# Performance work log

Hardware: AMD Instinct MI355X
Metric: run time of the kernel (lower is better)

## Reference

```python
import jax, jax.numpy as jnp
import numpy as np


def _spline(t, x):
    """Natural cubic spline second derivatives. t: (T,), x: (T, N, D)."""
    T = t.shape[0]
    h = jnp.diff(t)  # (T-1,)
    main = jnp.concatenate([jnp.ones((1,), t.dtype), 2.0 * (h[:-1] + h[1:]), jnp.ones((1,), t.dtype)])
    lower = jnp.concatenate([h[:-1], jnp.zeros((1,), t.dtype)])
    upper = jnp.concatenate([jnp.zeros((1,), t.dtype), h[1:]])
    A = jnp.diag(main) + jnp.diag(lower, -1) + jnp.diag(upper, 1)  # (T, T) tridiagonal, natural BCs
    slopes = (x[1:] - x[:-1]) / h[:, None, None]
    rhs = jnp.concatenate([jnp.zeros_like(x[:1]), 6.0 * (slopes[1:] - slopes[:-1]), jnp.zeros_like(x[:1])], 0)
    M = jnp.linalg.solve(A, rhs.reshape(T, -1)).reshape(x.shape)  # (T, N, D)
    return h, M


def setup_inputs() -> dict:
    key = jax.random.key(0)
    ks = jax.random.split(key, 8)
    B, Amax, T, D, E, H = 32, 64, 16, 10, 128, 512
    t = jnp.arange(T, dtype=jnp.float32)
    x = jax.random.normal(ks[0], (B, Amax, T, D), jnp.float32)
    mask = jax.random.randint(ks[1], (B, Amax), 0, 2) > 0

    def lin(k, o, i):
        k1, k2 = jax.random.split(k)
        s = 1.0 / float(np.sqrt(i))  # torch nn.Linear default init
        return (jax.random.uniform(k1, (o, i), jnp.float32, -s, s),
                jax.random.uniform(k2, (o,), jnp.float32, -s, s))

    W_embed, b_embed = lin(ks[2], E, D)
    W0, b0 = lin(ks[3], H, E)
    W1, b1 = lin(ks[4], H, H)
    W2, b2 = lin(ks[5], H, H)
    W3, b3 = lin(ks[6], E * D, H)
    return dict(t=t, x=x, mask=mask, W_embed=W_embed, b_embed=b_embed,
                W0=W0, b0=b0, W1=W1, b1=b1, W2=W2, b2=b2, W3=W3, b3=b3)


def reference(t, x, mask, W_embed, b_embed, W0, b0, W1, b1, W2, b2, W3, b3):
    B, Amax, T, D = x.shape
    E = W_embed.shape[0]
    xs = x.reshape(B * Amax, T, D).transpose(1, 0, 2)  # (T, N, D)
    h, M = _spline(t, xs)

    def dX_dt(s):
        # derivative of the natural cubic spline at scalar time s -> (N, D)
        i = jnp.clip(jnp.searchsorted(t, s, side='right') - 1, 0, T - 2)
        u = s - t[i]
        hi = h[i]
        b = (xs[i + 1] - xs[i]) / hi - hi * (2.0 * M[i] + M[i + 1]) / 6.0
        return b + M[i] * u + (M[i + 1] - M[i]) * (u * u) / (2.0 * hi)

    def f(z):
        # CDEFunc: linear-relu x3, linear, tanh, view (N, E, D)
        y = jax.nn.relu(z @ W0.T + b0)
        y = jax.nn.relu(y @ W1.T + b1)
        y = jax.nn.relu(y @ W2.T + b2)
        y = jnp.tanh(y @ W3.T + b3)
        return y.reshape(z.shape[0], E, D)

    def vf(s, z):
        # VectorField: f(z) @ dX_dt(s)  -> (N, E)
        return jnp.einsum('ned,nd->ne', f(z), dX_dt(s))

    # spline evaluated at the first knot is just the first observation
    z0 = xs[0] @ W_embed.T + b_embed  # (N, E)

    def step(z, ts):
        # torchdiffeq 'rk4' fixed-step solver (3/8-rule, rk4_alt_step_func)
        t0, t1 = ts
        hs = t1 - t0
        k1 = vf(t0, z)
        k2 = vf(t0 + hs / 3.0, z + hs * k1 / 3.0)
        k3 = vf(t0 + 2.0 * hs / 3.0, z + hs * (k2 - k1 / 3.0))
        k4 = vf(t1, z + hs * (k1 - k2 + k3))
        return z + hs * (k1 + 3.0 * (k2 + k3) + k4) / 8.0, None

    zT, _ = jax.lax.scan(step, z0, (t[:-1], t[1:]))
    # masked-out agents get an all-zero embedding (as in the torch scatter)
    return zT.reshape(B, Amax, E) * mask[..., None].astype(zT.dtype)
```

## Files before the change

kernel.cpp:

```cpp
#include <hip/hip_runtime.h>
#include <hip/hip_bf16.h>


typedef __attribute__((ext_vector_type(4))) float f32x4;
typedef __attribute__((ext_vector_type(8))) short s16x8;

#define N_AG  2048
#define D_IN  10
#define NPTS  46
#define RROWS 8

#define OFF_W0P 0
#define OFF_W1P (128 * 512)
#define OFF_W2P (OFF_W1P + 512 * 512)
#define OFF_W3P (OFF_W2P + 512 * 512)
#define OFF_END (OFF_W3P + 512 * 1280)

__device__ __forceinline__ ushort f2bf(float v) {
  __hip_bfloat16 h = __float2bfloat16(v);
  return *reinterpret_cast<ushort*>(&h);
}

__global__ void pack_w(const float* __restrict__ W, ushort* __restrict__ Wp,
                       int O, int K) {
  int idx = blockIdx.x * blockDim.x + threadIdx.x;
  if (idx >= O * K) return;
  int j    = idx & 7;
  int lane = (idx >> 3) & 63;
  int rest = idx >> 9;
  int KS   = K >> 5;
  int ks   = rest % KS;
  int ct   = rest / KS;
  int col  = (ct << 4) + (lane & 15);
  int k    = (ks << 5) + ((lane >> 4) << 3) + j;
  Wp[idx]  = f2bf(W[col * K + k]);
}

__global__ void spline_dx_k(const float* __restrict__ x, float* __restrict__ dX) {
  int idx = blockIdx.x * blockDim.x + threadIdx.x;
  if (idx >= N_AG * D_IN) return;
  int n = idx / D_IN;
  int d = idx - n * D_IN;

  float xv[16];
#pragma unroll
  for (int t = 0; t < 16; ++t) xv[t] = x[n * 160 + t * 10 + d];

  float cp[15], dp[15], M[16];
  {
    float rhs = 6.0f * (xv[2] - 2.0f * xv[1] + xv[0]);
    cp[1] = 0.25f;
    dp[1] = rhs * 0.25f;
#pragma unroll
    for (int i = 2; i <= 14; ++i) {
      rhs = 6.0f * (xv[i + 1] - 2.0f * xv[i] + xv[i - 1]);
      float m = 1.0f / (4.0f - cp[i - 1]);
      cp[i] = m;
      dp[i] = (rhs - dp[i - 1]) * m;
    }
    M[0] = 0.0f; M[15] = 0.0f;
    M[14] = dp[14];
#pragma unroll
    for (int i = 13; i >= 1; --i) M[i] = dp[i] - cp[i] * M[i + 1];
  }

#pragma unroll
  for (int p = 0; p < NPTS; ++p) {
    int i; float u;
    if (p < 45) { i = p / 3; u = (float)(p % 3) * (1.0f / 3.0f); }
    else        { i = 14;    u = 1.0f; }
    float b = (xv[i + 1] - xv[i]) - (2.0f * M[i] + M[i + 1]) * (1.0f / 6.0f);
    dX[p * (N_AG * D_IN) + idx] = b + M[i] * u + (M[i + 1] - M[i]) * (u * u * 0.5f);
  }
}

template <int KS, int NT, bool VF>
__device__ __forceinline__ void fc(const ushort* __restrict__ Ain, int arowb,
                                   const ushort* __restrict__ Wp,
                                   const float* __restrict__ bias_lds,
                                   ushort* __restrict__ Outb, int orowb,
                                   float (*__restrict__ vf)[128],
                                   const float (*__restrict__ dXs)[D_IN],
                                   int w, int lane, int tbase) {
  f32x4 acc[NT];
#pragma unroll
  for (int t = 0; t < NT; ++t) acc[t] = (f32x4){0.f, 0.f, 0.f, 0.f};

  const int row8 = lane & 7;
  const int g    = lane >> 4;
  const char* abase = (const char*)Ain + row8 * arowb;
  const int aswz = row8 << 4;

#pragma unroll 2
  for (int ks = 0; ks < KS; ++ks) {
    s16x8 a = *(const s16x8*)(abase + (((ks << 6) + (g << 4)) ^ aswz));
#pragma unroll
    for (int t = 0; t < NT; ++t) {
      int ct = w + ((tbase + t) << 3);
      s16x8 b = *(const s16x8*)(Wp + (((ct * KS + ks) * 64 + lane) << 3));
      acc[t] = __builtin_amdgcn_mfma_f32_16x16x32_bf16(a, b, acc[t], 0, 0, 0);
    }
  }

#pragma unroll
  for (int t = 0; t < NT; ++t) {
    int ct  = w + ((tbase + t) << 3);
    int col = (ct << 4) + (lane & 15);
    float bb = bias_lds[col];
#pragma unroll
    for (int r = 0; r < 4; ++r) {
      int orow = (g << 2) + r;
      if (orow < RROWS) {
        float v = acc[t][r] + bb;
        if (!VF) {
          v = fmaxf(v, 0.f);
          int byte = (orow * orowb + (col << 1)) ^ (orow << 4);
          *(ushort*)((char*)Outb + byte) = f2bf(v);
        } else {
          v = 1.0f - 2.0f * __builtin_amdgcn_rcpf(__expf(2.0f * v) + 1.0f);
          int e = col / 10, d = col - e * 10;
          atomicAdd(&vf[orow][e], v * dXs[orow][d]);
        }
      }
    }
  }
}

__global__ __launch_bounds__(512, 2) void cde_mfma(
    const float* __restrict__ x, const int* __restrict__ mask,
    const float* __restrict__ We, const float* __restrict__ be,
    const float* __restrict__ b0, const float* __restrict__ b1,
    const float* __restrict__ b2, const float* __restrict__ b3,
    const ushort* __restrict__ Wp, const float* __restrict__ dX,
    float* __restrict__ out) {
  const int tid  = threadIdx.x;
  const int lane = tid & 63;
  const int w    = tid >> 6;
  const int n0   = blockIdx.x * RROWS;

  __shared__ ushort A0[RROWS * 128];
  __shared__ ushort H1[RROWS * 512];
  __shared__ ushort H2[RROWS * 512];
  __shared__ float  BL[2816];
  __shared__ float  vf[RROWS][128];
  __shared__ float  dXs[RROWS][D_IN];

  float zreg[2], k1r[2], k2r[2], k3r[2];

  {
    int i = tid;
    BL[i] = b0[i]; BL[512 + i] = b1[i]; BL[1024 + i] = b2[i];
    BL[1536 + i] = b3[i];
    BL[2048 + i] = b3[512 + i];
    if (tid < 256) BL[2560 + tid] = b3[1024 + tid];
  }

#pragma unroll
  for (int q = 0; q < 2; ++q) {
    int idx = (q << 9) + tid;
    int e = idx & 127, row = idx >> 7;
    float acc = be[e];
    const float* xr = x + (n0 + row) * 160;
#pragma unroll
    for (int d = 0; d < 10; ++d) acc = fmaf(xr[d], We[e * 10 + d], acc);
    zreg[q] = acc;
    int byte = ((row << 8) + (e << 1)) ^ (row << 4);
    *(ushort*)((char*)A0 + byte) = f2bf(acc);
  }
  __syncthreads();

#pragma unroll 1
  for (int s = 0; s < 15; ++s) {
#pragma unroll 1
    for (int st = 0; st < 4; ++st) {
      if (tid < RROWS * D_IN) {
        int p = (st < 3) ? (3 * s + st) : ((s < 14) ? (3 * s + 3) : 45);
        dXs[tid / 10][tid % 10] = dX[p * (N_AG * D_IN) + n0 * 10 + tid];
      }
      fc<4, 2, false>(A0, 256, Wp + OFF_W0P, BL, H1, 1024, vf, dXs, w, lane, 0);
      fc<4, 2, false>(A0, 256, Wp + OFF_W0P, BL, H1, 1024, vf, dXs, w, lane, 2);
      __syncthreads();
      fc<16, 2, false>(H1, 1024, Wp + OFF_W1P, BL + 512, H2, 1024, vf, dXs, w, lane, 0);
      fc<16, 2, false>(H1, 1024, Wp + OFF_W1P, BL + 512, H2, 1024, vf, dXs, w, lane, 2);
      __syncthreads();
      fc<16, 2, false>(H2, 1024, Wp + OFF_W2P, BL + 1024, H1, 1024, vf, dXs, w, lane, 0);
      fc<16, 2, false>(H2, 1024, Wp + OFF_W2P, BL + 1024, H1, 1024, vf, dXs, w, lane, 2);
      ((float*)vf)[tid] = 0.f;
      ((float*)vf)[512 + tid] = 0.f;
      __syncthreads();
      fc<16, 5, true>(H1, 1024, Wp + OFF_W3P, BL + 1536, nullptr, 0, vf, dXs, w, lane, 0);
      fc<16, 5, true>(H1, 1024, Wp + OFF_W3P, BL + 1536, nullptr, 0, vf, dXs, w, lane, 5);
      __syncthreads();

#pragma unroll
      for (int q = 0; q < 2; ++q) {
        int idx = (q << 9) + tid;
        int e = idx & 127, row = idx >> 7;
        float dv = vf[row][e];
        float z = zreg[q], zin;
        if (st == 0)      { k1r[q] = dv; zin = z + dv * (1.f / 3.f); }
        else if (st == 1) { k2r[q] = dv; zin = z + dv - k1r[q] * (1.f / 3.f); }
        else if (st == 2) { k3r[q] = dv; zin = z + k1r[q] - k2r[q] + dv; }
        else {
          z += (k1r[q] + 3.f * (k2r[q] + k3r[q]) + dv) * 0.125f;
          zreg[q] = z; zin = z;
        }
        int byte = ((row << 8) + (e << 1)) ^ (row << 4);
        *(ushort*)((char*)A0 + byte) = f2bf(zin);
      }
      __syncthreads();
    }
  }

#pragma unroll
  for (int q = 0; q < 2; ++q) {
    int idx = (q << 9) + tid;
    int e = idx & 127, row = idx >> 7;
    out[(n0 + row) * 128 + e] = (mask[n0 + row] != 0) ? zreg[q] : 0.f;
  }
}

extern "C" void kernel_launch(void* const* d_in, const int* in_sizes, int n_in,
                              void* d_out, int out_size, void* d_ws, size_t ws_size,
                              hipStream_t stream) {
  const float* x    = (const float*)d_in[1];
  const int*   mask = (const int*)d_in[2];
  const float* We   = (const float*)d_in[3];
  const float* be   = (const float*)d_in[4];
  const float* W0   = (const float*)d_in[5];
  const float* b0   = (const float*)d_in[6];
  const float* W1   = (const float*)d_in[7];
  const float* b1   = (const float*)d_in[8];
  const float* W2   = (const float*)d_in[9];
  const float* b2   = (const float*)d_in[10];
  const float* W3   = (const float*)d_in[11];
  const float* b3   = (const float*)d_in[12];
  float* out = (float*)d_out;

  ushort* wp = (ushort*)d_ws;
  float*  dX = (float*)((char*)d_ws + (size_t)OFF_END * 2);

  pack_w<<<(128 * 512 + 255) / 256, 256, 0, stream>>>(W0, wp + OFF_W0P, 512, 128);
  pack_w<<<(512 * 512 + 255) / 256, 256, 0, stream>>>(W1, wp + OFF_W1P, 512, 512);
  pack_w<<<(512 * 512 + 255) / 256, 256, 0, stream>>>(W2, wp + OFF_W2P, 512, 512);
  pack_w<<<(512 * 1280 + 255) / 256, 256, 0, stream>>>(W3, wp + OFF_W3P, 1280, 512);
  spline_dx_k<<<(N_AG * D_IN + 255) / 256, 256, 0, stream>>>(x, dX);
  cde_mfma<<<256, 512, 0, stream>>>(x, mask, We, be, b0, b1, b2, b3, wp, dX, out);
}
```

Measured before the change: 2.430 ms.

## Double block size to 16 waves and replace atomics with LDS tanh buffer contraction

The fused MLP kernel now runs with 1024 threads per block (16 waves), so each wave owns half as many output column tiles per layer and each thread handles one (row, e) state element. The last layer no longer uses per-element LDS atomicAdd into the vector-field accumulator. Tanh outputs are written as bf16 into a new LDS buffer, and each thread then contracts 10 values against dX. This removes atomic contention but adds bf16 rounding of the tanh outputs, more LDS, and heavier register pressure under the 1024-thread launch bounds.

```diff
diff --git a/kernel.cpp b/kernel.cpp
--- a/kernel.cpp
+++ b/kernel.cpp
@@ -19,6 +19,9 @@
 __device__ __forceinline__ ushort f2bf(float v) {
   __hip_bfloat16 h = __float2bfloat16(v);
   return *reinterpret_cast<ushort*>(&h);
+}
+__device__ __forceinline__ float bf2f(ushort u) {
+  union { unsigned u; float f; } c; c.u = ((unsigned)u) << 16; return c.f;
 }
 
 __global__ void pack_w(const float* __restrict__ W, ushort* __restrict__ Wp,
@@ -74,13 +77,11 @@
   }
 }
 
-template <int KS, int NT, bool VF>
+template <int KS, int NT, bool RELU>
 __device__ __forceinline__ void fc(const ushort* __restrict__ Ain, int arowb,
                                    const ushort* __restrict__ Wp,
                                    const float* __restrict__ bias_lds,
                                    ushort* __restrict__ Outb, int orowb,
-                                   float (*__restrict__ vf)[128],
-                                   const float (*__restrict__ dXs)[D_IN],
                                    int w, int lane, int tbase) {
   f32x4 acc[NT];
 #pragma unroll
@@ -91,12 +92,12 @@
   const char* abase = (const char*)Ain + row8 * arowb;
   const int aswz = row8 << 4;
 
-#pragma unroll 2
+#pragma unroll 4
   for (int ks = 0; ks < KS; ++ks) {
     s16x8 a = *(const s16x8*)(abase + (((ks << 6) + (g << 4)) ^ aswz));
 #pragma unroll
     for (int t = 0; t < NT; ++t) {
-      int ct = w + ((tbase + t) << 3);
+      int ct = w + ((tbase + t) << 4);
       s16x8 b = *(const s16x8*)(Wp + (((ct * KS + ks) * 64 + lane) << 3));
       acc[t] = __builtin_amdgcn_mfma_f32_16x16x32_bf16(a, b, acc[t], 0, 0, 0);
     }
@@ -104,7 +105,7 @@
 
 #pragma unroll
   for (int t = 0; t < NT; ++t) {
-    int ct  = w + ((tbase + t) << 3);
+    int ct  = w + ((tbase + t) << 4);
     int col = (ct << 4) + (lane & 15);
     float bb = bias_lds[col];
 #pragma unroll
@@ -112,21 +113,16 @@
       int orow = (g << 2) + r;
       if (orow < RROWS) {
         float v = acc[t][r] + bb;
-        if (!VF) {
-          v = fmaxf(v, 0.f);
-          int byte = (orow * orowb + (col << 1)) ^ (orow << 4);
-          *(ushort*)((char*)Outb + byte) = f2bf(v);
-        } else {
-          v = 1.0f - 2.0f * __builtin_amdgcn_rcpf(__expf(2.0f * v) + 1.0f);
-          int e = col / 10, d = col - e * 10;
-          atomicAdd(&vf[orow][e], v * dXs[orow][d]);
-        }
+        if (RELU) v = fmaxf(v, 0.f);
+        else      v = 1.0f - 2.0f * __builtin_amdgcn_rcpf(__expf(2.0f * v) + 1.0f);
+        int byte = (orow * orowb + (col << 1)) ^ (orow << 4);
+        *(ushort*)((char*)Outb + byte) = f2bf(v);
       }
     }
   }
 }
 
-__global__ __launch_bounds__(512, 2) void cde_mfma(
+__global__ __launch_bounds__(1024, 4) void cde_mfma(
     const float* __restrict__ x, const int* __restrict__ mask,
     const float* __restrict__ We, const float* __restrict__ be,
     const float* __restrict__ b0, const float* __restrict__ b1,
@@ -141,29 +137,26 @@
   __shared__ ushort A0[RROWS * 128];
   __shared__ ushort H1[RROWS * 512];
   __shared__ ushort H2[RROWS * 512];
+  __shared__ ushort G[RROWS * 1280];
   __shared__ float  BL[2816];
-  __shared__ float  vf[RROWS][128];
   __shared__ float  dXs[RROWS][D_IN];
 
-  float zreg[2], k1r[2], k2r[2], k3r[2];
-
+  float zreg, k1r, k2r, k3r;
+
+  if (tid < 512) {
+    BL[tid] = b0[tid]; BL[512 + tid] = b1[tid]; BL[1024 + tid] = b2[tid];
+  }
+  BL[1536 + tid] = b3[tid];
+  if (tid < 256) BL[2560 + tid] = b3[1024 + tid];
+
+  const int e   = tid & 127;
+  const int row = tid >> 7;
   {
-    int i = tid;
-    BL[i] = b0[i]; BL[512 + i] = b1[i]; BL[1024 + i] = b2[i];
-    BL[1536 + i] = b3[i];
-    BL[2048 + i] = b3[512 + i];
-    if (tid < 256) BL[2560 + tid] = b3[1024 + tid];
-  }
-
-#pragma unroll
-  for (int q = 0; q < 2; ++q) {
-    int idx = (q << 9) + tid;
-    int e = idx & 127, row = idx >> 7;
     float acc = be[e];
     const float* xr = x + (n0 + row) * 160;
 #pragma unroll
     for (int d = 0; d < 10; ++d) acc = fmaf(xr[d], We[e * 10 + d], acc);
-    zreg[q] = acc;
+    zreg = acc;
     int byte = ((row << 8) + (e << 1)) ^ (row << 4);
     *(ushort*)((char*)A0 + byte) = f2bf(acc);
   }
@@ -177,33 +170,30 @@
         int p = (st < 3) ? (3 * s + st) : ((s < 14) ? (3 * s + 3) : 45);
         dXs[tid / 10][tid % 10] = dX[p * (N_AG * D_IN) + n0 * 10 + tid];
       }
-      fc<4, 2, false>(A0, 256, Wp + OFF_W0P, BL, H1, 1024, vf, dXs, w, lane, 0);
-      fc<4, 2, false>(A0, 256, Wp + OFF_W0P, BL, H1, 1024, vf, dXs, w, lane, 2);
-      __syncthreads();
-      fc<16, 2, false>(H1, 1024, Wp + OFF_W1P, BL + 512, H2, 1024, vf, dXs, w, lane, 0);
-      fc<16, 2, false>(H1, 1024, Wp + OFF_W1P, BL + 512, H2, 1024, vf, dXs, w, lane, 2);
-      __syncthreads();
-      fc<16, 2, false>(H2, 1024, Wp + OFF_W2P, BL + 1024, H1, 1024, vf, dXs, w, lane, 0);
-      fc<16, 2, false>(H2, 1024, Wp + OFF_W2P, BL + 1024, H1, 1024, vf, dXs, w, lane, 2);
-      ((float*)vf)[tid] = 0.f;
-      ((float*)vf)[512 + tid] = 0.f;
-      __syncthreads();
-      fc<16, 5, true>(H1, 1024, Wp + OFF_W3P, BL + 1536, nullptr, 0, vf, dXs, w, lane, 0);
-      fc<16, 5, true>(H1, 1024, Wp + OFF_W3P, BL + 1536, nullptr, 0, vf, dXs, w, lane, 5);
-      __syncthreads();
-
-#pragma unroll
-      for (int q = 0; q < 2; ++q) {
-        int idx = (q << 9) + tid;
-        int e = idx & 127, row = idx >> 7;
-        float dv = vf[row][e];
-        float z = zreg[q], zin;
-        if (st == 0)      { k1r[q] = dv; zin = z + dv * (1.f / 3.f); }
-        else if (st == 1) { k2r[q] = dv; zin = z + dv - k1r[q] * (1.f / 3.f); }
-        else if (st == 2) { k3r[q] = dv; zin = z + k1r[q] - k2r[q] + dv; }
+      fc<4, 2, true>(A0, 256, Wp + OFF_W0P, BL, H1, 1024, w, lane, 0);
+      __syncthreads();
+      fc<16, 2, true>(H1, 1024, Wp + OFF_W1P, BL + 512, H2, 1024, w, lane, 0);
+      __syncthreads();
+      fc<16, 2, true>(H2, 1024, Wp + OFF_W2P, BL + 1024, H1, 1024, w, lane, 0);
+      __syncthreads();
+      fc<16, 3, false>(H1, 1024, Wp + OFF_W3P, BL + 1536, G, 2560, w, lane, 0);
+      fc<16, 2, false>(H1, 1024, Wp + OFF_W3P, BL + 1536, G, 2560, w, lane, 3);
+      __syncthreads();
+
+      {
+        float dv = 0.f;
+#pragma unroll
+        for (int d = 0; d < 10; ++d) {
+          int byte = (row * 2560 + ((e * 10 + d) << 1)) ^ (row << 4);
+          dv = fmaf(bf2f(*(const ushort*)((const char*)G + byte)), dXs[row][d], dv);
+        }
+        float z = zreg, zin;
+        if (st == 0)      { k1r = dv; zin = z + dv * (1.f / 3.f); }
+        else if (st == 1) { k2r = dv; zin = z + dv - k1r * (1.f / 3.f); }
+        else if (st == 2) { k3r = dv; zin = z + k1r - k2r + dv; }
         else {
-          z += (k1r[q] + 3.f * (k2r[q] + k3r[q]) + dv) * 0.125f;
-          zreg[q] = z; zin = z;
+          z += (k1r + 3.f * (k2r + k3r) + dv) * 0.125f;
+          zreg = z; zin = z;
         }
         int byte = ((row << 8) + (e << 1)) ^ (row << 4);
         *(ushort*)((char*)A0 + byte) = f2bf(zin);
@@ -212,12 +202,7 @@
     }
   }
 
-#pragma unroll
-  for (int q = 0; q < 2; ++q) {
-    int idx = (q << 9) + tid;
-    int e = idx & 127, row = idx >> 7;
-    out[(n0 + row) * 128 + e] = (mask[n0 + row] != 0) ? zreg[q] : 0.f;
-  }
+  out[(n0 + row) * 128 + e] = (mask[n0 + row] != 0) ? zreg : 0.f;
 }
 
 extern "C" void kernel_launch(void* const* d_in, const int* in_sizes, int n_in,
@@ -245,5 +230,5 @@
   pack_w<<<(512 * 512 + 255) / 256, 256, 0, stream>>>(W2, wp + OFF_W2P, 512, 512);
   pack_w<<<(512 * 1280 + 255) / 256, 256, 0, stream>>>(W3, wp + OFF_W3P, 1280, 512);
   spline_dx_k<<<(N_AG * D_IN + 255) / 256, 256, 0, stream>>>(x, dX);
-  cde_mfma<<<256, 512, 0, stream>>>(x, mask, We, be, b0, b1, b2, b3, wp, dX, out);
-}
+  cde_mfma<<<256, 1024, 0, stream>>>(x, mask, We, be, b0, b1, b2, b3, wp, dX, out);
+}
```

Measured after the change: 3.027 ms. 1.25x slower.
